# Kernel optimization log

Hardware: AMD Instinct MI355X
Metric: run time of the kernel (lower is better)

The kernel has to match this reference:

```python
import jax, jax.numpy as jnp
import numpy as np

ITERATIONS = 3

def setup_inputs() -> dict:
    key = jax.random.key(0)
    k1, k2 = jax.random.split(key)
    C, S, H = 64, 128, 2048
    x = jax.random.normal(k1, (C, S, H), dtype=jnp.float32)
    W = jax.random.normal(k2, (H, H), dtype=jnp.float32)
    return {"x": x, "W": W}

def reference(x, W):
    # x: [C, S, H], W: [H, H]
    C, S, H = x.shape
    # e_ij is loop-invariant in the original; hoist it (same math, computed once)
    e_ij = jnp.einsum('csh,hk->csk', x, W)  # [C, S, H]
    b_ij = jnp.zeros((C, S), dtype=x.dtype)
    c_i = jnp.zeros((C, H), dtype=x.dtype)
    for _ in range(ITERATIONS):
        d_i = jax.nn.softmax(b_ij, axis=1)[:, :, None]          # [C, S, 1], softmax over S
        c_i = jnp.sum(d_i * e_ij, axis=1)                        # [C, H]
        squared = jnp.sum(c_i ** 2, axis=1, keepdims=True)       # [C, 1]
        coeff = squared / (1.0 + squared) / jnp.sqrt(squared + 1e-9)
        c_i = coeff * c_i                                        # squash
        b_ij = b_ij + jnp.einsum('csh,ch->cs', e_ij, c_i)        # logit update
    return c_i
```

## Files before the change

kernel.cpp:

```cpp
#include <hip/hip_runtime.h>

using bf16x8 = __attribute__((ext_vector_type(8))) __bf16;
using f32x4  = __attribute__((ext_vector_type(4))) float;

#define C_ 64
#define S_ 128
#define H_ 2048
#define M_ 8192

__device__ __forceinline__ unsigned short f2bf(float f) {
  unsigned u = __float_as_uint(f);
  u = u + 0x7fffu + ((u >> 16) & 1u);
  return (unsigned short)(u >> 16);
}
__device__ __forceinline__ float bf2f(unsigned short h) {
  return __uint_as_float(((unsigned)h) << 16);
}

__device__ __forceinline__ void glds16(const unsigned short* g, unsigned short* l) {
  __builtin_amdgcn_global_load_lds(
      (const __attribute__((address_space(1))) void*)g,
      (__attribute__((address_space(3))) void*)l, 16, 0, 0);
}

__global__ void k_split_all(const float* __restrict__ x,
                            unsigned short* __restrict__ xh,
                            unsigned short* __restrict__ xl,
                            const float* __restrict__ W,
                            unsigned short* __restrict__ Wth,
                            unsigned short* __restrict__ Wtl,
                            float* __restrict__ G) {
  __shared__ float Ts[64][68];
  const int b = blockIdx.x;
  const int t = threadIdx.x;
  if (b < 16384) {
    int idx = b * 256 + t;
    float4 v = ((const float4*)x)[idx];
    float a[4] = {v.x, v.y, v.z, v.w};
    unsigned short h[4], l[4];
#pragma unroll
    for (int q = 0; q < 4; ++q) {
      h[q] = f2bf(a[q]);
      l[q] = f2bf(a[q] - bf2f(h[q]));
    }
    ((ushort4*)xh)[idx] = make_ushort4(h[0], h[1], h[2], h[3]);
    ((ushort4*)xl)[idx] = make_ushort4(l[0], l[1], l[2], l[3]);
  } else if (b < 17408) {
    const int bb = b - 16384;
    const int k0 = (bb & 31) * 64, n0 = (bb >> 5) * 64;
#pragma unroll
    for (int p = 0; p < 4; ++p) {
      int idx = t + p * 256;
      int r = idx >> 4, c4 = (idx & 15) * 4;
      *(float4*)&Ts[r][c4] = *(const float4*)(W + (size_t)(k0 + r) * H_ + n0 + c4);
    }
    __syncthreads();
#pragma unroll
    for (int p = 0; p < 4; ++p) {
      int idx = t + p * 256;
      int rr = idx >> 4, cc = (idx & 15) * 4;
      unsigned short h[4], l[4];
#pragma unroll
      for (int q = 0; q < 4; ++q) {
        float f = Ts[cc + q][rr];
        h[q] = f2bf(f);
        l[q] = f2bf(f - bf2f(h[q]));
      }
      size_t o = (size_t)(n0 + rr) * H_ + k0 + cc;
      *(ushort4*)(Wth + o) = make_ushort4(h[0], h[1], h[2], h[3]);
      *(ushort4*)(Wtl + o) = make_ushort4(l[0], l[1], l[2], l[3]);
    }
  } else {
    const int bb = b - 17408;
    ((float4*)G)[bb * 256 + t] = (float4){0.f, 0.f, 0.f, 0.f};
  }
}

#define TILE_USH 24576
#define OFF_AH 0
#define OFF_AL 8192
#define OFF_BH 16384
#define OFF_BL 20480

__global__ __launch_bounds__(512, 2) void k_gemm3(
    const unsigned short* __restrict__ Ah, const unsigned short* __restrict__ Al,
    const unsigned short* __restrict__ Bh, const unsigned short* __restrict__ Bl,
    unsigned short* __restrict__ Eh, unsigned short* __restrict__ El) {
  __shared__ unsigned short lds[3 * TILE_USH];
  const int t = threadIdx.x;
  const int lane = t & 63, wid = t >> 6;
  const int wm = wid >> 1, wn = wid & 1;
  const int l16 = lane & 15, quad = lane >> 4;

  const int lin = blockIdx.x + (blockIdx.y << 5);
  const int xcd = lin & 7, slot = lin >> 3;
  const int bm = ((xcd >> 1) << 3) + (slot >> 3);
  const int bn = ((xcd & 1) << 3) + (slot & 7);

  const int rl = lane >> 2;
  const int gg8 = (((lane & 3) ^ ((rl >> 1) & 3)) << 3);
  const unsigned short* gAh0 = Ah + (size_t)(bm * 256 + wid * 16 + rl) * H_ + gg8;
  const unsigned short* gAl0 = Al + (size_t)(bm * 256 + wid * 16 + rl) * H_ + gg8;
  const unsigned short* gAh1 = gAh0 + (size_t)128 * H_;
  const unsigned short* gAl1 = gAl0 + (size_t)128 * H_;
  const unsigned short* gBh  = Bh + (size_t)(bn * 128 + wid * 16 + rl) * H_ + gg8;
  const unsigned short* gBl  = Bl + (size_t)(bn * 128 + wid * 16 + rl) * H_ + gg8;
  const int dA0 = wid * 512;
  const int dA1 = dA0 + 4096;
  const int dB  = wid * 512;

  const int colq = ((quad ^ ((l16 >> 1) & 3)) << 3);
  const int rA = (wm * 64 + l16) * 32 + colq;
  const int rB = (wn * 64 + l16) * 32 + colq;

  f32x4 acc[4][4];
#pragma unroll
  for (int i = 0; i < 4; ++i)
#pragma unroll
    for (int j = 0; j < 4; ++j) acc[i][j] = (f32x4)0.f;

  auto stage6 = [&](int bo, int k) {
    glds16(gAh0 + k, &lds[bo + OFF_AH + dA0]);
    glds16(gAh1 + k, &lds[bo + OFF_AH + dA1]);
    glds16(gAl0 + k, &lds[bo + OFF_AL + dA0]);
    glds16(gAl1 + k, &lds[bo + OFF_AL + dA1]);
    glds16(gBh + k,  &lds[bo + OFF_BH + dB]);
    glds16(gBl + k,  &lds[bo + OFF_BL + dB]);
  };

  auto body = [&](int co, int n2o, int k2, bool issue) {
    bf16x8 ah[4], al[4], bh[4], bl[4];
    if (issue) {
      glds16(gAh0 + k2, &lds[n2o + OFF_AH + dA0]);
      glds16(gAl0 + k2, &lds[n2o + OFF_AL + dA0]);
      glds16(gBh + k2,  &lds[n2o + OFF_BH + dB]);
    }
#pragma unroll
    for (int i = 0; i < 4; ++i) {
      ah[i] = *(const bf16x8*)&lds[co + OFF_AH + rA + i * 512];
      al[i] = *(const bf16x8*)&lds[co + OFF_AL + rA + i * 512];
    }
#pragma unroll
    for (int j = 0; j < 2; ++j) {
      bh[j] = *(const bf16x8*)&lds[co + OFF_BH + rB + j * 512];
      bl[j] = *(const bf16x8*)&lds[co + OFF_BL + rB + j * 512];
    }
    __builtin_amdgcn_s_barrier();
    asm volatile("s_waitcnt lgkmcnt(0)" ::: "memory");
    __builtin_amdgcn_sched_barrier(0);
    __builtin_amdgcn_s_setprio(1);
#pragma unroll
    for (int i = 0; i < 4; ++i)
#pragma unroll
      for (int j = 0; j < 2; ++j) {
        acc[i][j] = __builtin_amdgcn_mfma_f32_16x16x32_bf16(ah[i], bh[j], acc[i][j], 0, 0, 0);
        acc[i][j] = __builtin_amdgcn_mfma_f32_16x16x32_bf16(ah[i], bl[j], acc[i][j], 0, 0, 0);
        acc[i][j] = __builtin_amdgcn_mfma_f32_16x16x32_bf16(al[i], bh[j], acc[i][j], 0, 0, 0);
      }
    __builtin_amdgcn_s_setprio(0);
    __builtin_amdgcn_s_barrier();
    if (issue) {
      glds16(gAh1 + k2, &lds[n2o + OFF_AH + dA1]);
      glds16(gAl1 + k2, &lds[n2o + OFF_AL + dA1]);
      glds16(gBl + k2,  &lds[n2o + OFF_BL + dB]);
    }
#pragma unroll
    for (int j = 2; j < 4; ++j) {
      bh[j] = *(const bf16x8*)&lds[co + OFF_BH + rB + j * 512];
      bl[j] = *(const bf16x8*)&lds[co + OFF_BL + rB + j * 512];
    }
    __builtin_amdgcn_s_barrier();
    asm volatile("s_waitcnt lgkmcnt(0)" ::: "memory");
    __builtin_amdgcn_sched_barrier(0);
    __builtin_amdgcn_s_setprio(1);
#pragma unroll
    for (int i = 0; i < 4; ++i)
#pragma unroll
      for (int j = 2; j < 4; ++j) {
        acc[i][j] = __builtin_amdgcn_mfma_f32_16x16x32_bf16(ah[i], bh[j], acc[i][j], 0, 0, 0);
        acc[i][j] = __builtin_amdgcn_mfma_f32_16x16x32_bf16(ah[i], bl[j], acc[i][j], 0, 0, 0);
        acc[i][j] = __builtin_amdgcn_mfma_f32_16x16x32_bf16(al[i], bh[j], acc[i][j], 0, 0, 0);
      }
    __builtin_amdgcn_s_setprio(0);
    if (issue) asm volatile("s_waitcnt vmcnt(6)" ::: "memory");
    else       asm volatile("s_waitcnt vmcnt(0)" ::: "memory");
    __builtin_amdgcn_s_barrier();
  };

  stage6(0, 0);
  stage6(TILE_USH, 32);
  asm volatile("s_waitcnt vmcnt(6)" ::: "memory");
  __builtin_amdgcn_s_barrier();

  int cur = 0;
#pragma unroll 1
  for (int tt = 0; tt < 62; ++tt) {
    int n2 = cur + 2; if (n2 >= 3) n2 -= 3;
    body(cur * TILE_USH, n2 * TILE_USH, (tt + 2) * 32, true);
    cur = (cur == 2) ? 0 : cur + 1;
  }
  body(cur * TILE_USH, 0, 0, false);
  cur = (cur == 2) ? 0 : cur + 1;
  body(cur * TILE_USH, 0, 0, false);

#pragma unroll
  for (int i = 0; i < 4; ++i) {
    const int row0 = bm * 256 + wm * 64 + i * 16 + quad * 4;
#pragma unroll
    for (int j = 0; j < 4; ++j) {
      const int col = bn * 128 + wn * 64 + j * 16 + l16;
#pragma unroll
      for (int r = 0; r < 4; ++r) {
        float v = acc[i][j][r];
        unsigned short hh = f2bf(v);
        unsigned short ll = f2bf(v - bf2f(hh));
        Eh[(size_t)(row0 + r) * H_ + col] = hh;
        El[(size_t)(row0 + r) * H_ + col] = ll;
      }
    }
  }
}

__global__ __launch_bounds__(256, 4) void k_gram_mfma(
    const unsigned short* __restrict__ Eh, const unsigned short* __restrict__ El,
    float* __restrict__ G) {
  __shared__ unsigned short sH[128 * 32], sL[128 * 32];
  const int t = threadIdx.x;
  const int kc = blockIdx.x;
  const int cc = blockIdx.y;
  const int lane = t & 63, wid = t >> 6;
  const int wm = wid >> 1, wn = wid & 1;
  const int l16 = lane & 15, quad = lane >> 4;

  const int rl = lane >> 2;
  const int gg = (lane & 3) ^ ((rl >> 1) & 3);
  const int c0 = wid * 2, c1 = c0 + 1;
  const unsigned short* gH0 = Eh + (size_t)(cc * 128 + c0 * 16 + rl) * H_ + gg * 8;
  const unsigned short* gH1 = Eh + (size_t)(cc * 128 + c1 * 16 + rl) * H_ + gg * 8;
  const unsigned short* gL0 = El + (size_t)(cc * 128 + c0 * 16 + rl) * H_ + gg * 8;
  const unsigned short* gL1 = El + (size_t)(cc * 128 + c1 * 16 + rl) * H_ + gg * 8;
  unsigned short* lH0 = sH + c0 * 512;
  unsigned short* lH1 = sH + c1 * 512;
  unsigned short* lL0 = sL + c0 * 512;
  unsigned short* lL1 = sL + c1 * 512;

  const int swz = ((l16 >> 1) & 3);
  const int colq = ((quad ^ swz) * 8);

  f32x4 acc[4][4];
#pragma unroll
  for (int i = 0; i < 4; ++i)
#pragma unroll
    for (int j = 0; j < 4; ++j) acc[i][j] = (f32x4)0.f;

  const int kbeg = kc * 512;
  for (int k0 = kbeg; k0 < kbeg + 512; k0 += 32) {
    __syncthreads();
    glds16(gH0 + k0, lH0);
    glds16(gH1 + k0, lH1);
    glds16(gL0 + k0, lL0);
    glds16(gL1 + k0, lL1);
    __syncthreads();

    bf16x8 ah[4], al[4], bh[4], bl[4];
#pragma unroll
    for (int i = 0; i < 4; ++i) {
      const int ra = (wm * 64 + i * 16 + l16) * 32;
      const int rb = (wn * 64 + i * 16 + l16) * 32;
      ah[i] = *(const bf16x8*)&sH[ra + colq];
      al[i] = *(const bf16x8*)&sL[ra + colq];
      bh[i] = *(const bf16x8*)&sH[rb + colq];
      bl[i] = *(const bf16x8*)&sL[rb + colq];
    }
#pragma unroll
    for (int i = 0; i < 4; ++i)
#pragma unroll
      for (int j = 0; j < 4; ++j) {
        acc[i][j] = __builtin_amdgcn_mfma_f32_16x16x32_bf16(ah[i], bh[j], acc[i][j], 0, 0, 0);
        acc[i][j] = __builtin_amdgcn_mfma_f32_16x16x32_bf16(ah[i], bl[j], acc[i][j], 0, 0, 0);
        acc[i][j] = __builtin_amdgcn_mfma_f32_16x16x32_bf16(al[i], bh[j], acc[i][j], 0, 0, 0);
      }
  }

  float* Gc = G + (size_t)cc * S_ * S_;
#pragma unroll
  for (int i = 0; i < 4; ++i) {
    const int row0 = wm * 64 + i * 16 + quad * 4;
#pragma unroll
    for (int j = 0; j < 4; ++j) {
      const int col = wn * 64 + j * 16 + l16;
#pragma unroll
      for (int r = 0; r < 4; ++r)
        atomicAdd(&Gc[(row0 + r) * S_ + col], acc[i][j][r]);
    }
  }
}

__global__ void k_out2(const unsigned short* __restrict__ Eh,
                       const unsigned short* __restrict__ El,
                       const float* __restrict__ G, float* __restrict__ out) {
  const int c = blockIdx.y;
  const int s = threadIdx.x & 127;
  __shared__ float dsh[128];
  __shared__ float red[128];
  __shared__ float wsh[128];
  const float* Gc = G + (size_t)c * S_ * S_;
  float b = 0.f;
  for (int it = 0; it < 3; ++it) {
    red[s] = b; __syncthreads();
    for (int off = 64; off > 0; off >>= 1) {
      if (s < off) red[s] = fmaxf(red[s], red[s + off]);
      __syncthreads();
    }
    float mx = red[0]; __syncthreads();
    float ev = expf(b - mx);
    red[s] = ev; __syncthreads();
    for (int off = 64; off > 0; off >>= 1) {
      if (s < off) red[s] = red[s] + red[s + off];
      __syncthreads();
    }
    float Z = red[0]; __syncthreads();
    float d = ev / Z;
    dsh[s] = d; __syncthreads();
    float y = 0.f;
#pragma unroll 8
    for (int j = 0; j < S_; ++j) y = fmaf(Gc[j * S_ + s], dsh[j], y);
    red[s] = d * y; __syncthreads();
    for (int off = 64; off > 0; off >>= 1) {
      if (s < off) red[s] = red[s] + red[s + off];
      __syncthreads();
    }
    float sq = red[0]; __syncthreads();
    float coeff = sq / (1.f + sq) / sqrtf(sq + 1e-9f);
    if (it == 2) wsh[s] = coeff * d;
    else b += coeff * y;
  }
  __syncthreads();

  const int h2 = blockIdx.x * 256 + threadIdx.x;
  const unsigned* Ph = (const unsigned*)(Eh + (size_t)c * S_ * H_) + h2;
  const unsigned* Pl = (const unsigned*)(El + (size_t)c * S_ * H_) + h2;
  float a0 = 0.f, a1 = 0.f;
#pragma unroll 8
  for (int ss = 0; ss < S_; ++ss) {
    unsigned uh = Ph[(size_t)ss * (H_ / 2)];
    unsigned ul = Pl[(size_t)ss * (H_ / 2)];
    a0 = fmaf(wsh[ss], bf2f((unsigned short)uh) + bf2f((unsigned short)ul), a0);
    a1 = fmaf(wsh[ss], bf2f((unsigned short)(uh >> 16)) + bf2f((unsigned short)(ul >> 16)), a1);
  }
  ((float2*)(out + (size_t)c * H_))[h2] = make_float2(a0, a1);
}

extern "C" void kernel_launch(void* const* d_in, const int* in_sizes, int n_in,
                              void* d_out, int out_size, void* d_ws, size_t ws_size,
                              hipStream_t stream) {
  (void)in_sizes; (void)n_in; (void)out_size; (void)ws_size;
  const float* x = (const float*)d_in[0];
  const float* W = (const float*)d_in[1];
  float* out = (float*)d_out;
  char* ws = (char*)d_ws;

  unsigned short* xh  = (unsigned short*)(ws);
  unsigned short* xl  = (unsigned short*)(ws + 33554432);
  unsigned short* Wth = (unsigned short*)(ws + 67108864);
  unsigned short* Wtl = (unsigned short*)(ws + 75497472);
  unsigned short* Eh  = (unsigned short*)(ws + 83886080);
  unsigned short* El  = (unsigned short*)(ws + 117440512);
  float*          G   = (float*)(ws + 150994944);

  k_split_all<<<dim3(18432), 256, 0, stream>>>(x, xh, xl, W, Wth, Wtl, G);
  k_gemm3<<<dim3(32, 16), 512, 0, stream>>>(xh, xl, Wth, Wtl, Eh, El);
  k_gram_mfma<<<dim3(4, 64), 256, 0, stream>>>(Eh, El, G);
  k_out2<<<dim3(4, 64), 256, 0, stream>>>(Eh, El, G, out);
}
```

Before: 347.4 us.

## Simplify GEMM main loop to one barrier per K-tile with bulk prefetch

Replaces the two-phase K-tile body, which split LDS reads, global-to-LDS prefetches and MFMA work into halves separated by several barriers, with a single phase per tile. Each iteration reads all A/B fragments, issues all six prefetch loads for tile t+2, runs all 48 MFMAs, waits on vmcnt and hits one barrier. This cuts barrier and waitcnt overhead but gives up the finer interleaving of loads and MFMAs and holds all fragments live at once, which raises register pressure. The explicit lgkmcnt wait and sched_barrier are gone, so the compiler now schedules the LDS reads itself.

```diff
diff --git a/kernel.cpp b/kernel.cpp
--- a/kernel.cpp
+++ b/kernel.cpp
@@ -128,80 +128,42 @@
     glds16(gBl + k,  &lds[bo + OFF_BL + dB]);
   };
 
-  auto body = [&](int co, int n2o, int k2, bool issue) {
+  stage6(0, 0);
+  stage6(TILE_USH, 32);
+  asm volatile("s_waitcnt vmcnt(6)" ::: "memory");
+  __builtin_amdgcn_s_barrier();
+
+  int cur = 0;
+#pragma unroll 1
+  for (int tt = 0; tt < 64; ++tt) {
+    const int co = cur * TILE_USH;
     bf16x8 ah[4], al[4], bh[4], bl[4];
-    if (issue) {
-      glds16(gAh0 + k2, &lds[n2o + OFF_AH + dA0]);
-      glds16(gAl0 + k2, &lds[n2o + OFF_AL + dA0]);
-      glds16(gBh + k2,  &lds[n2o + OFF_BH + dB]);
-    }
 #pragma unroll
     for (int i = 0; i < 4; ++i) {
       ah[i] = *(const bf16x8*)&lds[co + OFF_AH + rA + i * 512];
       al[i] = *(const bf16x8*)&lds[co + OFF_AL + rA + i * 512];
-    }
-#pragma unroll
-    for (int j = 0; j < 2; ++j) {
-      bh[j] = *(const bf16x8*)&lds[co + OFF_BH + rB + j * 512];
-      bl[j] = *(const bf16x8*)&lds[co + OFF_BL + rB + j * 512];
-    }
-    __builtin_amdgcn_s_barrier();
-    asm volatile("s_waitcnt lgkmcnt(0)" ::: "memory");
-    __builtin_amdgcn_sched_barrier(0);
+      bh[i] = *(const bf16x8*)&lds[co + OFF_BH + rB + i * 512];
+      bl[i] = *(const bf16x8*)&lds[co + OFF_BL + rB + i * 512];
+    }
+    if (tt < 62) {
+      int n2 = cur + 2; if (n2 >= 3) n2 -= 3;
+      stage6(n2 * TILE_USH, (tt + 2) * 32);
+    }
     __builtin_amdgcn_s_setprio(1);
 #pragma unroll
     for (int i = 0; i < 4; ++i)
 #pragma unroll
-      for (int j = 0; j < 2; ++j) {
+      for (int j = 0; j < 4; ++j) {
         acc[i][j] = __builtin_amdgcn_mfma_f32_16x16x32_bf16(ah[i], bh[j], acc[i][j], 0, 0, 0);
         acc[i][j] = __builtin_amdgcn_mfma_f32_16x16x32_bf16(ah[i], bl[j], acc[i][j], 0, 0, 0);
         acc[i][j] = __builtin_amdgcn_mfma_f32_16x16x32_bf16(al[i], bh[j], acc[i][j], 0, 0, 0);
       }
     __builtin_amdgcn_s_setprio(0);
-    __builtin_amdgcn_s_barrier();
-    if (issue) {
-      glds16(gAh1 + k2, &lds[n2o + OFF_AH + dA1]);
-      glds16(gAl1 + k2, &lds[n2o + OFF_AL + dA1]);
-      glds16(gBl + k2,  &lds[n2o + OFF_BL + dB]);
-    }
-#pragma unroll
-    for (int j = 2; j < 4; ++j) {
-      bh[j] = *(const bf16x8*)&lds[co + OFF_BH + rB + j * 512];
-      bl[j] = *(const bf16x8*)&lds[co + OFF_BL + rB + j * 512];
-    }
-    __builtin_amdgcn_s_barrier();
-    asm volatile("s_waitcnt lgkmcnt(0)" ::: "memory");
-    __builtin_amdgcn_sched_barrier(0);
-    __builtin_amdgcn_s_setprio(1);
-#pragma unroll
-    for (int i = 0; i < 4; ++i)
-#pragma unroll
-      for (int j = 2; j < 4; ++j) {
-        acc[i][j] = __builtin_amdgcn_mfma_f32_16x16x32_bf16(ah[i], bh[j], acc[i][j], 0, 0, 0);
-        acc[i][j] = __builtin_amdgcn_mfma_f32_16x16x32_bf16(ah[i], bl[j], acc[i][j], 0, 0, 0);
-        acc[i][j] = __builtin_amdgcn_mfma_f32_16x16x32_bf16(al[i], bh[j], acc[i][j], 0, 0, 0);
-      }
-    __builtin_amdgcn_s_setprio(0);
-    if (issue) asm volatile("s_waitcnt vmcnt(6)" ::: "memory");
-    else       asm volatile("s_waitcnt vmcnt(0)" ::: "memory");
-    __builtin_amdgcn_s_barrier();
-  };
-
-  stage6(0, 0);
-  stage6(TILE_USH, 32);
-  asm volatile("s_waitcnt vmcnt(6)" ::: "memory");
-  __builtin_amdgcn_s_barrier();
-
-  int cur = 0;
-#pragma unroll 1
-  for (int tt = 0; tt < 62; ++tt) {
-    int n2 = cur + 2; if (n2 >= 3) n2 -= 3;
-    body(cur * TILE_USH, n2 * TILE_USH, (tt + 2) * 32, true);
-    cur = (cur == 2) ? 0 : cur + 1;
-  }
-  body(cur * TILE_USH, 0, 0, false);
-  cur = (cur == 2) ? 0 : cur + 1;
-  body(cur * TILE_USH, 0, 0, false);
+    if (tt < 62)       asm volatile("s_waitcnt vmcnt(6)" ::: "memory");
+    else if (tt == 62) asm volatile("s_waitcnt vmcnt(0)" ::: "memory");
+    if (tt < 63) __builtin_amdgcn_s_barrier();
+    cur = cur + 1; if (cur == 3) cur = 0;
+  }
 
 #pragma unroll
   for (int i = 0; i < 4; ++i) {
```

Measured after the change: 342.9 us. No clear change (-1.3%).
